# Optimization experiments

Hardware: AMD Instinct MI355X
Metric: run time of the kernel (lower is better)

Reference implementation:

```python
import jax, jax.numpy as jnp
import numpy as np

BUCKET_SIZE = 64
N_HASHES = 8
SELF_ATTN_VALUE = -5e4  # TOKEN_SELF_ATTN_VALUE
EPS = 1e-12  # F.normalize eps


def setup_inputs() -> dict:
    key = jax.random.key(0)
    k1, k2, k3 = jax.random.split(key, 3)
    B, S, D = 16, 4096, 128
    n_buckets = S // BUCKET_SIZE  # 64
    qk = jax.random.normal(k1, (B, S, D), dtype=jnp.float32)
    v = jax.random.normal(k2, (B, S, D), dtype=jnp.float32)
    # rotations_shape = (1, dim, n_hashes, n_buckets // 2); shared across batch
    rotations = jax.random.normal(k3, (1, D, N_HASHES, n_buckets // 2), dtype=jnp.float32)
    return {"qk": qk, "v": v, "rotations": rotations}


def _hash_vectors(qk, rotations, n_buckets):
    # qk: (B,S,D), rotations: (1,D,H,n_buckets//2)
    rotated = jnp.einsum('btf,fhi->bhti', qk, rotations[0])  # (B,H,S,nb/2)
    rotated = jnp.concatenate([rotated, -rotated], axis=-1)   # (B,H,S,nb)
    buckets = jnp.argmax(rotated, axis=-1)                    # (B,H,S)
    offsets = (jnp.arange(N_HASHES) * n_buckets)[None, :, None]
    return (buckets + offsets).reshape(qk.shape[0], -1)       # (B, H*S)


def _look_one_back(x):
    # concat each chunk with its predecessor (circular), along the window dim
    return jnp.concatenate([x, jnp.roll(x, 1, axis=1)], axis=2)


def reference(qk, v, rotations):
    B, S, D = qk.shape
    H = N_HASHES
    n_buckets = S // BUCKET_SIZE
    buckets = _hash_vectors(qk, rotations, n_buckets)         # (B, H*S) int

    ticker = jnp.broadcast_to(jnp.arange(H * S)[None, :], (B, H * S))
    buckets_and_t = S * buckets + (ticker % S)                # unique keys
    sticker = jnp.argsort(buckets_and_t, axis=-1)             # sort by bucket
    undo_sort = jnp.argsort(sticker, axis=-1)

    st = sticker % S                                          # original positions
    sqk = jnp.take_along_axis(qk, st[..., None], axis=1)      # (B,H*S,D)
    sv = jnp.take_along_axis(v, st[..., None], axis=1)

    C = H * n_buckets                                         # num chunks
    bq_t = st.reshape(B, C, -1)                               # (B,C,w)
    bqk = sqk.reshape(B, C, -1, D)
    bv = sv.reshape(B, C, -1, D)
    bq = bqk
    nrm = jnp.maximum(jnp.linalg.norm(bqk, axis=-1, keepdims=True), EPS)
    bk = bqk / nrm                                            # F.normalize

    bk = _look_one_back(bk)                                   # (B,C,2w,D)
    bv = _look_one_back(bv)
    bkv_t = _look_one_back(bq_t)                              # (B,C,2w)

    dots = jnp.einsum('bcie,bcje->bcij', bq, bk) * (D ** -0.5)  # (B,C,w,2w)
    self_mask = bq_t[:, :, :, None] == bkv_t[:, :, None, :]
    dots = jnp.where(self_mask, SELF_ATTN_VALUE, dots)

    lse = jax.scipy.special.logsumexp(dots, axis=-1, keepdims=True)
    probs = jnp.exp(dots - lse)
    bo = jnp.einsum('bcij,bcje->bcie', probs, bv)             # (B,C,w,D)

    so = bo.reshape(B, -1, D)                                 # (B,H*S,D)
    slogits = lse.reshape(B, -1)                              # (B,H*S)
    o = jnp.take_along_axis(so, undo_sort[..., None], axis=1)
    logits = jnp.take_along_axis(slogits, undo_sort, axis=1)

    o = o.reshape(B, H, S, D)
    logits = logits.reshape(B, H, S, 1)
    w = jnp.exp(logits - jax.scipy.special.logsumexp(logits, axis=1, keepdims=True))
    out = jnp.sum(o * w, axis=1)                              # (B,S,D)
    return out
```

## Files before the change

### kernel.cpp

```cpp
#include <hip/hip_runtime.h>
#include <hip/hip_bf16.h>


#define B_ 16
#define S_ 4096
#define D_ 128
#define H_ 8
#define C_ 512
#define SCALE_ 0.08838834764831845f

typedef __attribute__((ext_vector_type(8))) short bf16x8;
typedef __attribute__((ext_vector_type(8))) _Float16 f16x8;
typedef __attribute__((ext_vector_type(2))) _Float16 f16x2t;
typedef __attribute__((ext_vector_type(4))) float f32x4;
typedef __attribute__((ext_vector_type(2))) float f32x2v;
typedef __attribute__((ext_vector_type(4))) int int4v;

union BF8U { int4v i; bf16x8 b; };
union F16x8U { int4v i; f16x8 h; };

__device__ __forceinline__ unsigned hi_pack(float x0, float x1) {
    unsigned a, b;
    __builtin_memcpy(&b, &x0, 4);
    __builtin_memcpy(&a, &x1, 4);
    return __builtin_amdgcn_perm(a, b, 0x07060302u);
}
__device__ __forceinline__ float truncbf(float x) {
    unsigned u; __builtin_memcpy(&u, &x, 4);
    u &= 0xFFFF0000u;
    float f; __builtin_memcpy(&f, &u, 4);
    return f;
}
__device__ __forceinline__ unsigned pack2f16(float x0, float x1) {
    f16x2t h = {(_Float16)x0, (_Float16)x1};
    unsigned u; __builtin_memcpy(&u, &h, 4);
    return u;
}

__global__ __launch_bounds__(256) void norm_kernel(const float* __restrict__ qk,
                                                   float* __restrict__ rnrm) {
    int half = threadIdx.x >> 5;
    int lane32 = threadIdx.x & 31;
    size_t row = (size_t)blockIdx.x * 8 + half;
    float4 vv = ((const float4*)(qk + row * D_))[lane32];
    float ss = vv.x * vv.x + vv.y * vv.y + vv.z * vv.z + vv.w * vv.w;
    #pragma unroll
    for (int m = 1; m < 32; m <<= 1) ss += __shfl_xor(ss, m, 64);
    if (lane32 == 0) rnrm[row] = 1.0f / fmaxf(sqrtf(ss), 1e-12f);
}

__global__ __launch_bounds__(256) void prep_rot_kernel(const float* __restrict__ rot,
                                                       short* __restrict__ rth,
                                                       short* __restrict__ rtl) {
    int x = blockIdx.x * 256 + threadIdx.x;
    int hp = x >> 11;
    int ia = (x >> 5) & 63;
    int ft = x & 31;
    float v0 = rot[(size_t)(ft * 4 + 0) * 256 + hp * 64 + ia];
    float v1 = rot[(size_t)(ft * 4 + 1) * 256 + hp * 64 + ia];
    float v2 = rot[(size_t)(ft * 4 + 2) * 256 + hp * 64 + ia];
    float v3 = rot[(size_t)(ft * 4 + 3) * 256 + hp * 64 + ia];
    unsigned h0 = hi_pack(v0, v1), h1 = hi_pack(v2, v3);
    unsigned l0 = hi_pack(v0 - truncbf(v0), v1 - truncbf(v1));
    unsigned l1 = hi_pack(v2 - truncbf(v2), v3 - truncbf(v3));
    int off = ia * 128 + ((((ft >> 1) ^ (ia & 7)) << 3) | ((ft & 1) << 2));
    *(int2*)&rth[hp * 8192 + off] = make_int2((int)h0, (int)h1);
    *(int2*)&rtl[hp * 8192 + off] = make_int2((int)l0, (int)l1);
}

__global__ __launch_bounds__(256) void hash_kernel(const float* __restrict__ qk,
                                                   const float* __restrict__ rot,
                                                   const short* __restrict__ rth,
                                                   const short* __restrict__ rtl,
                                                   int* __restrict__ buckets) {
    __shared__ unsigned char flags[8][64];

    const int b = blockIdx.x >> 6;
    const int tile = blockIdx.x & 63;
    const int tid = threadIdx.x;
    const int w = tid >> 6, l = tid & 63, g = l >> 4, m = l & 15;

    if (tid < 32) ((int4*)flags)[tid] = make_int4(0, 0, 0, 0);
    __syncthreads();

    const float* qrow = qk + ((size_t)b * S_ + (size_t)tile * 64 + w * 16 + m) * D_;
    bf16x8 qh[4], qlr[4];
    #pragma unroll
    for (int s = 0; s < 4; ++s) {
        float4 xa = *(const float4*)(qrow + s * 32 + g * 8);
        float4 xb = *(const float4*)(qrow + s * 32 + g * 8 + 4);
        BF8U hu, lu;
        hu.i[0] = (int)hi_pack(xa.x, xa.y); hu.i[1] = (int)hi_pack(xa.z, xa.w);
        hu.i[2] = (int)hi_pack(xb.x, xb.y); hu.i[3] = (int)hi_pack(xb.z, xb.w);
        lu.i[0] = (int)hi_pack(xa.x - truncbf(xa.x), xa.y - truncbf(xa.y));
        lu.i[1] = (int)hi_pack(xa.z - truncbf(xa.z), xa.w - truncbf(xa.w));
        lu.i[2] = (int)hi_pack(xb.x - truncbf(xb.x), xb.y - truncbf(xb.y));
        lu.i[3] = (int)hi_pack(xb.z - truncbf(xb.z), xb.w - truncbf(xb.w));
        qh[s] = hu.b; qlr[s] = lu.b;
    }

    #pragma unroll
    for (int hp = 0; hp < 4; ++hp) {
        f32x4 dots_n[4];
        #pragma unroll
        for (int nt = 0; nt < 4; ++nt) {
            f32x4 acc = (f32x4){0.f, 0.f, 0.f, 0.f};
            #pragma unroll
            for (int s = 0; s < 4; ++s) {
                int kr = hp * 8192 + (nt * 16 + m) * 128 + (((s * 4 + g) ^ (m & 7)) << 3);
                bf16x8 bh = *(const bf16x8*)&rth[kr];
                bf16x8 bl = *(const bf16x8*)&rtl[kr];
                acc = __builtin_amdgcn_mfma_f32_16x16x32_bf16(qh[s], bh, acc, 0, 0, 0);
                acc = __builtin_amdgcn_mfma_f32_16x16x32_bf16(qh[s], bl, acc, 0, 0, 0);
                acc = __builtin_amdgcn_mfma_f32_16x16x32_bf16(qlr[s], bh, acc, 0, 0, 0);
            }
            dots_n[nt] = acc;
        }

        #pragma unroll
        for (int hh = 0; hh < 2; ++hh) {
            int h = hp * 2 + hh;
            #pragma unroll
            for (int r = 0; r < 4; ++r) {
                float v1 = -1e30f, v2 = -1e30f; int i1 = 0;
                #pragma unroll
                for (int nn = 0; nn < 2; ++nn) {
                    float v = dots_n[hh * 2 + nn][r];
                    int i = nn * 16 + m;
                    if (v > v1 || (v == v1 && i < i1)) { v2 = v1; v1 = v; i1 = i; }
                    else v2 = fmaxf(v2, v);
                    float nv = -v; int ni = i + 32;
                    if (nv > v1 || (nv == v1 && ni < i1)) { v2 = v1; v1 = nv; i1 = ni; }
                    else v2 = fmaxf(v2, nv);
                }
                #pragma unroll
                for (int mask = 1; mask <= 8; mask <<= 1) {
                    float ov1 = __shfl_xor(v1, mask, 64);
                    int   oi1 = __shfl_xor(i1, mask, 64);
                    float ov2 = __shfl_xor(v2, mask, 64);
                    bool takeOther = (ov1 > v1) || (ov1 == v1 && oi1 < i1);
                    float loser = takeOther ? v1 : ov1;
                    float nv1 = takeOther ? ov1 : v1;
                    int   ni1 = takeOther ? oi1 : i1;
                    v2 = fmaxf(fmaxf(v2, ov2), loser);
                    v1 = nv1; i1 = ni1;
                }
                if (m == 0) {
                    int tok = w * 16 + g * 4 + r;
                    if (v1 - v2 < 2e-2f) flags[h][tok] = 1;
                    buckets[(((size_t)(b * H_ + h)) << 12) + tile * 64 + tok] = i1;
                }
            }
        }
    }
    __syncthreads();

    int tok = tid >> 2, part = tid & 3;
    const float* qtok = qk + ((size_t)b * S_ + (size_t)tile * 64 + tok) * D_;
    for (int h = 0; h < H_; ++h) {
        if (!flags[h][tok]) continue;
        double pd[8] = {0, 0, 0, 0, 0, 0, 0, 0};
        #pragma unroll 2
        for (int f = 0; f < 128; ++f) {
            double q = (double)qtok[f];
            const float* rp = rot + (size_t)f * 256 + h * 32 + part * 8;
            float4 r0 = *(const float4*)rp;
            float4 r1 = *(const float4*)(rp + 4);
            pd[0] = fma(q, (double)r0.x, pd[0]);
            pd[1] = fma(q, (double)r0.y, pd[1]);
            pd[2] = fma(q, (double)r0.z, pd[2]);
            pd[3] = fma(q, (double)r0.w, pd[3]);
            pd[4] = fma(q, (double)r1.x, pd[4]);
            pd[5] = fma(q, (double)r1.y, pd[5]);
            pd[6] = fma(q, (double)r1.z, pd[6]);
            pd[7] = fma(q, (double)r1.w, pd[7]);
        }
        double bv = -1e300; int bi = 0;
        #pragma unroll
        for (int ii = 0; ii < 8; ++ii) {
            int i = part * 8 + ii;
            double v = pd[ii];
            if (v > bv || (v == bv && i < bi)) { bv = v; bi = i; }
            double nv = -v; int ni = i + 32;
            if (nv > bv || (nv == bv && ni < bi)) { bv = nv; bi = ni; }
        }
        #pragma unroll
        for (int mm = 1; mm <= 2; mm <<= 1) {
            double ov = __shfl_xor(bv, mm, 64);
            int oi = __shfl_xor(bi, mm, 64);
            if (ov > bv || (ov == bv && oi < bi)) { bv = ov; bi = oi; }
        }
        if (part == 0) buckets[(((size_t)(b * H_ + h)) << 12) + tile * 64 + tok] = bi;
    }
}

__global__ __launch_bounds__(256) void sort_kernel(const int* __restrict__ buckets,
                                                   int* __restrict__ st,
                                                   int* __restrict__ inv,
                                                   const float* __restrict__ rnrm,
                                                   float* __restrict__ rnrm_s) {
    __shared__ unsigned short hist[256][64];
    __shared__ int base[64];
    __shared__ int totals[64];
    int tid = threadIdx.x;
    const int* bkrow = buckets + (size_t)blockIdx.x * S_;
    const float* rnb = rnrm + (size_t)(blockIdx.x >> 3) * S_;

    unsigned int* h32 = (unsigned int*)hist;
    #pragma unroll
    for (int u = 0; u < 32; ++u) h32[u * 256 + tid] = 0;
    __syncthreads();

    #pragma unroll
    for (int u = 0; u < 16; ++u) {
        int t = tid * 16 + u;
        int bk = bkrow[t];
        hist[tid][bk]++;
    }
    __syncthreads();

    if (tid < 64) {
        int bucket = tid;
        int run = 0;
        for (int ch = 0; ch < 256; ++ch) {
            int v = hist[ch][bucket];
            hist[ch][bucket] = (unsigned short)run;
            run += v;
        }
        totals[bucket] = run;
    }
    __syncthreads();
    if (tid == 0) {
        int acc = 0;
        for (int k = 0; k < 64; ++k) { base[k] = acc; acc += totals[k]; }
    }
    __syncthreads();

    int* strow = st + (size_t)blockIdx.x * S_;
    int* invrow = inv + (size_t)blockIdx.x * S_;
    float* rnsrow = rnrm_s + (size_t)blockIdx.x * S_;
    #pragma unroll
    for (int u = 0; u < 16; ++u) {
        int t = tid * 16 + u;
        int bk = bkrow[t];
        int off = hist[tid][bk];
        hist[tid][bk] = (unsigned short)(off + 1);
        int pos = base[bk] + off;
        strow[pos] = t;
        invrow[t] = pos;
        rnsrow[pos] = rnb[t] * SCALE_;
    }
}

__device__ __forceinline__ void transpose4(const float4 v, int g, float (&w_)[4]) {
    bool b0 = (g & 1) != 0, b1 = (g & 2) != 0;
    float k0 = b1 ? v.z : v.x;
    float k1 = b1 ? v.w : v.y;
    float s0 = b1 ? v.x : v.z;
    float s1 = b1 ? v.y : v.w;
    float r0 = __shfl_xor(s0, 32, 64);
    float r1 = __shfl_xor(s1, 32, 64);
    float kq_ = b0 ? k1 : k0;
    float rq_ = b0 ? r1 : r0;
    float sk  = b0 ? k0 : k1;
    float sr  = b0 ? r0 : r1;
    float tk_ = __shfl_xor(sk, 16, 64);
    float tr_ = __shfl_xor(sr, 16, 64);
    float A0 = b0 ? tk_ : kq_;
    float A1 = b0 ? kq_ : tk_;
    float B0 = b0 ? tr_ : rq_;
    float B1 = b0 ? rq_ : tr_;
    w_[0] = b1 ? B0 : A0;
    w_[1] = b1 ? B1 : A1;
    w_[2] = b1 ? A0 : B0;
    w_[3] = b1 ? A1 : B1;
}

template<bool DENSE>
__global__ __launch_bounds__(256, 4) void attn_mfma_kernel(
        const float* __restrict__ qk, const float* __restrict__ rnrm_s,
        const float* __restrict__ vglob, const int* __restrict__ st,
        float* __restrict__ outnum, float* __restrict__ den,
        _Float16* __restrict__ snum, float* __restrict__ sden) {
    __shared__ int tq_s[64];
    __shared__ int tk1_s[64];
    __shared__ float rns0[64];
    __shared__ float rns1[64];
    __shared__ short kbuf[8192];
    __shared__ short vbuf[8192];

    const int p = blockIdx.x;
    const int bc = (p & 7) * 1024 + (p >> 3);
    const int b  = bc >> 9;
    const int c  = bc & 511;
    const int tid = threadIdx.x;
    const int w   = tid >> 6;
    const int l   = tid & 63;
    const int g   = l >> 4;
    const int m   = l & 15;
    const size_t bS = ((size_t)b << 12);
    const int* stb = st + ((size_t)b << 15);

    const int c1 = (c + 511) & 511;
    if (tid < 64) {
        tq_s[tid]  = stb[c * 64 + tid];
        tk1_s[tid] = stb[c1 * 64 + tid];
        rns0[tid] = rnrm_s[(((size_t)(b * H_ + (c >> 6))) << 12) + (size_t)(c & 63) * 64 + tid];
        rns1[tid] = rnrm_s[(((size_t)(b * H_ + (c1 >> 6))) << 12) + (size_t)(c1 & 63) * 64 + tid];
    }
    __syncthreads();

    const int qtok_m = tq_s[w * 16 + m];

    f16x8 qh[4];
    f32x4 e4[4];
    f32x4 acc_o[8];
    #pragma unroll
    for (int dt = 0; dt < 8; ++dt) acc_o[dt] = (f32x4){0.f, 0.f, 0.f, 0.f};
    float densum = 0.0f;

    float4 kreg[8];
    float4 va[4], vb[4];

    auto issue_k = [&](const int* __restrict__ toks) {
        #pragma unroll
        for (int u = 0; u < 8; ++u) {
            int token = u * 8 + (tid >> 5);
            int cc = tid & 31;
            kreg[u] = *(const float4*)(qk + (bS + toks[token]) * D_ + cc * 4);
        }
    };
    auto write_k = [&]() {
        #pragma unroll
        for (int u = 0; u < 8; ++u) {
            int token = u * 8 + (tid >> 5);
            int cc = tid & 31;
            float4 vv = kreg[u];
            unsigned h0 = pack2f16(vv.x, vv.y), h1 = pack2f16(vv.z, vv.w);
            int kw = token * 128 + ((((cc >> 1) ^ (token & 7)) << 3) | ((cc & 1) << 2));
            *(int2*)&kbuf[kw] = make_int2((int)h0, (int)h1);
        }
    };
    auto issue_v = [&](const int* __restrict__ toks) {
        #pragma unroll
        for (int up = 0; up < 4; ++up) {
            int kq8 = w * 16 + (up & 1) * 8;
            int cc = (up >> 1) * 16 + m;
            va[up] = *(const float4*)(vglob + (bS + toks[kq8 + g]) * D_ + cc * 4);
            vb[up] = *(const float4*)(vglob + (bS + toks[kq8 + 4 + g]) * D_ + cc * 4);
        }
    };
    auto write_v = [&]() {
        #pragma unroll
        for (int up = 0; up < 4; ++up) {
            int kq8 = w * 16 + (up & 1) * 8;
            int cc = (up >> 1) * 16 + m;
            float wa[4], wb[4];
            transpose4(va[up], g, wa);
            transpose4(vb[up], g, wb);
            unsigned h0 = pack2f16(wa[0], wa[1]), h1 = pack2f16(wa[2], wa[3]);
            unsigned h2 = pack2f16(wb[0], wb[1]), h3 = pack2f16(wb[2], wb[3]);
            int d = cc * 4 + g;
            int ds = d ^ ((d >> 3) & 7);
            int kg = kq8 >> 3;
            int idx = (kg * 128 + ds) * 8;
            *(int4*)&vbuf[idx] = make_int4((int)h0, (int)h1, (int)h2, (int)h3);
        }
    };
    auto qk_pass = [&](int mode, const float* __restrict__ rns,
                       const int* __restrict__ tkp) {
        #pragma unroll
        for (int kt = 0; kt < 4; ++kt) {
            f32x4 acc = (f32x4){0.f, 0.f, 0.f, 0.f};
            #pragma unroll
            for (int s4 = 0; s4 < 4; ++s4) {
                int kr = (kt * 16 + m) * 128 + (((s4 * 4 + g) ^ (m & 7)) << 3);
                f16x8 ah = *(const f16x8*)&kbuf[kr];
                acc = __builtin_amdgcn_mfma_f32_16x16x32_f16(ah, qh[s4], acc, 0, 0, 0);
            }
            f32x4 rn4 = *(const f32x4*)&rns[kt * 16 + g * 4];
            int4v kt4;
            if (mode == 1) kt4 = *(const int4v*)&tkp[kt * 16 + g * 4];
            f32x4 e;
            #pragma unroll
            for (int r = 0; r < 4; ++r) {
                float ev = __expf(acc[r] * rn4[r]);
                if (mode == 0) {
                    if (kt == w && (g * 4 + r) == m) ev = 0.0f;
                } else {
                    if (kt4[r] == qtok_m) ev = 0.0f;
                }
                e[r] = ev;
                densum += ev;
            }
            e4[kt] = e;
        }
    };
    auto pv_pass = [&]() {
        #pragma unroll
        for (int s = 0; s < 2; ++s) {
            float pav[8];
            #pragma unroll
            for (int c2 = 0; c2 < 2; ++c2) {
                int srcLane = ((g & 1) * 2 + c2) * 16 + m;
                #pragma unroll
                for (int r = 0; r < 4; ++r) {
                    float v0 = __shfl(e4[2 * s][r], srcLane, 64);
                    float v1 = __shfl(e4[2 * s + 1][r], srcLane, 64);
                    pav[c2 * 4 + r] = (g >> 1) ? v1 : v0;
                }
            }
            F16x8U pahu;
            #pragma unroll
            for (int j2 = 0; j2 < 4; ++j2)
                pahu.i[j2] = (int)pack2f16(pav[2 * j2], pav[2 * j2 + 1]);
            f16x8 pah = pahu.h;
            #pragma unroll
            for (int dt = 0; dt < 8; ++dt) {
                int d = dt * 16 + m;
                int ds = d ^ ((d >> 3) & 7);
                int base = ((s * 4 + g) * 128 + ds) * 8;
                f16x8 vh = *(const f16x8*)&vbuf[base];
                acc_o[dt] = __builtin_amdgcn_mfma_f32_16x16x32_f16(pah, vh, acc_o[dt], 0, 0, 0);
            }
        }
    };

    issue_k(tq_s);
    write_k();
    __syncthreads();

    #pragma unroll
    for (int s4 = 0; s4 < 4; ++s4) {
        int qr = (w * 16 + m) * 128 + (((s4 * 4 + g) ^ (m & 7)) << 3);
        qh[s4] = *(const f16x8*)&kbuf[qr];
    }
    issue_v(tq_s);
    qk_pass(0, rns0, tq_s);
    write_v();
    __syncthreads();

    issue_k(tk1_s);
    pv_pass();
    write_k();
    __syncthreads();

    issue_v(tk1_s);
    qk_pass(1, rns1, tk1_s);
    write_v();
    __syncthreads();

    pv_pass();

    densum += __shfl_xor(densum, 16, 64);
    densum += __shfl_xor(densum, 32, 64);

    if (DENSE) {
        const int h = c >> 6;
        const size_t base = (((size_t)(b * H_ + h)) << 12) + (size_t)(c & 63) * 64;
        #pragma unroll
        for (int r = 0; r < 4; ++r) {
            int row = w * 16 + g * 4 + r;
            _Float16* nrow = snum + (base + row) * D_;
            #pragma unroll
            for (int dt = 0; dt < 8; ++dt)
                __builtin_nontemporal_store((_Float16)acc_o[dt][r], nrow + dt * 16 + m);
        }
        if (g == 0) __builtin_nontemporal_store(densum, sden + base + w * 16 + m);
    } else {
        if (g == 0) atomicAdd(den + bS + qtok_m, densum);
        int4v q4tok = *(const int4v*)&tq_s[w * 16 + g * 4];
        #pragma unroll
        for (int r = 0; r < 4; ++r) {
            float* obase = outnum + ((bS + q4tok[r]) * D_);
            #pragma unroll
            for (int dt = 0; dt < 8; ++dt)
                atomicAdd(obase + dt * 16 + m, acc_o[dt][r]);
        }
    }
}

__global__ __launch_bounds__(256) void combine_kernel(
        const _Float16* __restrict__ snum, const float* __restrict__ sden,
        const int* __restrict__ inv, float* __restrict__ out) {
    int wv = threadIdx.x >> 6, l = threadIdx.x & 63;
    int t = blockIdx.x * 4 + wv;
    int b = t >> 12, s = t & 4095;
    float s0 = 0.f, s1 = 0.f, dsum = 0.f;
    #pragma unroll
    for (int h = 0; h < H_; ++h) {
        int bh = b * H_ + h;
        int pos = inv[((size_t)bh << 12) + s];
        size_t row = ((size_t)bh << 12) + pos;
        dsum += __builtin_nontemporal_load(sden + row);
        unsigned uv = __builtin_nontemporal_load(
            (const unsigned*)(snum + row * D_ + 2 * l));
        unsigned short us0 = (unsigned short)(uv & 0xFFFFu);
        unsigned short us1 = (unsigned short)(uv >> 16);
        _Float16 h0, h1;
        __builtin_memcpy(&h0, &us0, 2);
        __builtin_memcpy(&h1, &us1, 2);
        s0 += (float)h0;
        s1 += (float)h1;
    }
    float rd = 1.0f / dsum;
    f32x2v o2 = {s0 * rd, s1 * rd};
    __builtin_nontemporal_store(o2, (f32x2v*)(out + (size_t)t * D_ + 2 * l));
}

__global__ __launch_bounds__(256) void div_kernel(float* __restrict__ out,
                                                  const float* __restrict__ den) {
    int i = blockIdx.x * 256 + threadIdx.x;
    float4 o = ((float4*)out)[i];
    float dn = den[i >> 5];
    ((float4*)out)[i] = make_float4(o.x / dn, o.y / dn, o.z / dn, o.w / dn);
}

extern "C" void kernel_launch(void* const* d_in, const int* in_sizes, int n_in,
                              void* d_out, int out_size, void* d_ws, size_t ws_size,
                              hipStream_t stream) {
    const float* qk  = (const float*)d_in[0];
    const float* v   = (const float*)d_in[1];
    const float* rot = (const float*)d_in[2];
    float* out = (float*)d_out;

    char* ws = (char*)d_ws;
    float* rnrm    = (float*)ws;
    int* buckets   = (int*)(ws + 262144);
    int* inv       = buckets;
    int* st        = (int*)(ws + 2359296);
    float* rnrm_s  = (float*)(ws + 4456448);
    float* sden    = (float*)(ws + 6553600);
    short* rth     = (short*)(ws + 8650752);
    short* rtl     = (short*)(ws + 8716288);
    _Float16* snum = (_Float16*)(ws + 8781824);
    const size_t need = 8781824ull + 134217728ull;

    norm_kernel<<<B_ * S_ / 8, 256, 0, stream>>>(qk, rnrm);
    prep_rot_kernel<<<32, 256, 0, stream>>>(rot, rth, rtl);
    hash_kernel<<<B_ * (S_ / 64), 256, 0, stream>>>(qk, rot, rth, rtl, buckets);
    sort_kernel<<<B_ * H_, 256, 0, stream>>>(buckets, st, inv, rnrm, rnrm_s);

    if (ws_size >= need) {
        attn_mfma_kernel<true><<<B_ * C_, 256, 0, stream>>>(
            qk, rnrm_s, v, st, nullptr, nullptr, snum, sden);
        combine_kernel<<<B_ * S_ / 4, 256, 0, stream>>>(snum, sden, inv, out);
    } else {
        float* den = sden;
        hipMemsetAsync(out, 0, (size_t)B_ * S_ * D_ * 4, stream);
        hipMemsetAsync(den, 0, (size_t)B_ * S_ * 4, stream);
        attn_mfma_kernel<false><<<B_ * C_, 256, 0, stream>>>(
            qk, rnrm_s, v, st, out, den, nullptr, nullptr);
        div_kernel<<<B_ * S_ * D_ / 4 / 256, 256, 0, stream>>>(out, den);
    }
}
```

Before: 274.4 us.

## Split hash kernel across hash pairs and pack argmax into 64-bit keys

The hash kernel now launches four times as many blocks, each handling one pair of hashes for a 64-token tile instead of all eight hashes, which raises parallelism and lets occupancy hints apply. The top-2 argmax reduction is rewritten to use order-preserving 64-bit packed keys (value plus inverted index), so each shuffle step moves two 64-bit values instead of three separate float/int values and compares them without branches. The cost is that every block reloads and re-splits the same qk tile into bf16 hi/lo parts, so qk reads and conversion work are repeated four times.

```diff
diff --git a/kernel.cpp b/kernel.cpp
--- a/kernel.cpp
+++ b/kernel.cpp
@@ -35,6 +35,14 @@
     f16x2t h = {(_Float16)x0, (_Float16)x1};
     unsigned u; __builtin_memcpy(&u, &h, 4);
     return u;
+}
+__device__ __forceinline__ unsigned enc_ks(unsigned u) {
+    return (u & 0x80000000u) ? ~u : (u | 0x80000000u);
+}
+__device__ __forceinline__ float dec_ks(unsigned ks) {
+    unsigned u = (ks & 0x80000000u) ? (ks ^ 0x80000000u) : ~ks;
+    float f; __builtin_memcpy(&f, &u, 4);
+    return f;
 }
 
 __global__ __launch_bounds__(256) void norm_kernel(const float* __restrict__ qk,
@@ -68,19 +76,20 @@
     *(int2*)&rtl[hp * 8192 + off] = make_int2((int)l0, (int)l1);
 }
 
-__global__ __launch_bounds__(256) void hash_kernel(const float* __restrict__ qk,
-                                                   const float* __restrict__ rot,
-                                                   const short* __restrict__ rth,
-                                                   const short* __restrict__ rtl,
-                                                   int* __restrict__ buckets) {
-    __shared__ unsigned char flags[8][64];
-
-    const int b = blockIdx.x >> 6;
-    const int tile = blockIdx.x & 63;
+__global__ __launch_bounds__(256, 4) void hash_kernel(
+        const float* __restrict__ qk, const float* __restrict__ rot,
+        const short* __restrict__ rth, const short* __restrict__ rtl,
+        int* __restrict__ buckets) {
+    __shared__ unsigned char flags[2][64];
+
+    const int bid = blockIdx.x;
+    const int b = bid >> 8;
+    const int tile = (bid >> 2) & 63;
+    const int hp = bid & 3;
     const int tid = threadIdx.x;
     const int w = tid >> 6, l = tid & 63, g = l >> 4, m = l & 15;
 
-    if (tid < 32) ((int4*)flags)[tid] = make_int4(0, 0, 0, 0);
+    if (tid < 8) ((int4*)flags)[tid] = make_int4(0, 0, 0, 0);
     __syncthreads();
 
     const float* qrow = qk + ((size_t)b * S_ + (size_t)tile * 64 + w * 16 + m) * D_;
@@ -99,57 +108,57 @@
         qh[s] = hu.b; qlr[s] = lu.b;
     }
 
-    #pragma unroll
-    for (int hp = 0; hp < 4; ++hp) {
-        f32x4 dots_n[4];
-        #pragma unroll
-        for (int nt = 0; nt < 4; ++nt) {
-            f32x4 acc = (f32x4){0.f, 0.f, 0.f, 0.f};
-            #pragma unroll
-            for (int s = 0; s < 4; ++s) {
-                int kr = hp * 8192 + (nt * 16 + m) * 128 + (((s * 4 + g) ^ (m & 7)) << 3);
-                bf16x8 bh = *(const bf16x8*)&rth[kr];
-                bf16x8 bl = *(const bf16x8*)&rtl[kr];
-                acc = __builtin_amdgcn_mfma_f32_16x16x32_bf16(qh[s], bh, acc, 0, 0, 0);
-                acc = __builtin_amdgcn_mfma_f32_16x16x32_bf16(qh[s], bl, acc, 0, 0, 0);
-                acc = __builtin_amdgcn_mfma_f32_16x16x32_bf16(qlr[s], bh, acc, 0, 0, 0);
-            }
-            dots_n[nt] = acc;
-        }
-
-        #pragma unroll
-        for (int hh = 0; hh < 2; ++hh) {
-            int h = hp * 2 + hh;
-            #pragma unroll
-            for (int r = 0; r < 4; ++r) {
-                float v1 = -1e30f, v2 = -1e30f; int i1 = 0;
-                #pragma unroll
-                for (int nn = 0; nn < 2; ++nn) {
-                    float v = dots_n[hh * 2 + nn][r];
-                    int i = nn * 16 + m;
-                    if (v > v1 || (v == v1 && i < i1)) { v2 = v1; v1 = v; i1 = i; }
-                    else v2 = fmaxf(v2, v);
-                    float nv = -v; int ni = i + 32;
-                    if (nv > v1 || (nv == v1 && ni < i1)) { v2 = v1; v1 = nv; i1 = ni; }
-                    else v2 = fmaxf(v2, nv);
-                }
-                #pragma unroll
-                for (int mask = 1; mask <= 8; mask <<= 1) {
-                    float ov1 = __shfl_xor(v1, mask, 64);
-                    int   oi1 = __shfl_xor(i1, mask, 64);
-                    float ov2 = __shfl_xor(v2, mask, 64);
-                    bool takeOther = (ov1 > v1) || (ov1 == v1 && oi1 < i1);
-                    float loser = takeOther ? v1 : ov1;
-                    float nv1 = takeOther ? ov1 : v1;
-                    int   ni1 = takeOther ? oi1 : i1;
-                    v2 = fmaxf(fmaxf(v2, ov2), loser);
-                    v1 = nv1; i1 = ni1;
-                }
-                if (m == 0) {
-                    int tok = w * 16 + g * 4 + r;
-                    if (v1 - v2 < 2e-2f) flags[h][tok] = 1;
-                    buckets[(((size_t)(b * H_ + h)) << 12) + tile * 64 + tok] = i1;
-                }
+    f32x4 dots_n[4];
+    #pragma unroll
+    for (int nt = 0; nt < 4; ++nt) {
+        f32x4 acc = (f32x4){0.f, 0.f, 0.f, 0.f};
+        #pragma unroll
+        for (int s = 0; s < 4; ++s) {
+            int kr = hp * 8192 + (nt * 16 + m) * 128 + (((s * 4 + g) ^ (m & 7)) << 3);
+            bf16x8 bh = *(const bf16x8*)&rth[kr];
+            bf16x8 bl = *(const bf16x8*)&rtl[kr];
+            acc = __builtin_amdgcn_mfma_f32_16x16x32_bf16(qh[s], bh, acc, 0, 0, 0);
+            acc = __builtin_amdgcn_mfma_f32_16x16x32_bf16(qh[s], bl, acc, 0, 0, 0);
+            acc = __builtin_amdgcn_mfma_f32_16x16x32_bf16(qlr[s], bh, acc, 0, 0, 0);
+        }
+        dots_n[nt] = acc;
+    }
+
+    #pragma unroll
+    for (int hh = 0; hh < 2; ++hh) {
+        int h = hp * 2 + hh;
+        #pragma unroll
+        for (int r = 0; r < 4; ++r) {
+            unsigned long long kM = 0ull, kS = 0ull;
+            #pragma unroll
+            for (int nn = 0; nn < 2; ++nn) {
+                float v = dots_n[hh * 2 + nn][r];
+                unsigned u; __builtin_memcpy(&u, &v, 4);
+                int i = nn * 16 + m;
+                unsigned long long kp =
+                    ((unsigned long long)enc_ks(u) << 6) | (unsigned)(63 - i);
+                unsigned long long kn =
+                    ((unsigned long long)enc_ks(u ^ 0x80000000u) << 6) |
+                    (unsigned)(63 - (i + 32));
+                if (kp > kM) { kS = kM; kM = kp; } else if (kp > kS) kS = kp;
+                if (kn > kM) { kS = kM; kM = kn; } else if (kn > kS) kS = kn;
+            }
+            #pragma unroll
+            for (int st = 1; st <= 8; st <<= 1) {
+                unsigned long long oM = __shfl_xor(kM, st, 64);
+                unsigned long long oS = __shfl_xor(kS, st, 64);
+                unsigned long long lo = kM < oM ? kM : oM;
+                kM = kM > oM ? kM : oM;
+                unsigned long long hs = kS > oS ? kS : oS;
+                kS = hs > lo ? hs : lo;
+            }
+            if (m == 0) {
+                int tok = w * 16 + g * 4 + r;
+                int i1 = 63 - (int)(kM & 63ull);
+                float v1 = dec_ks((unsigned)(kM >> 6));
+                float v2 = dec_ks((unsigned)(kS >> 6));
+                if (v1 - v2 < 2e-2f) flags[hh][tok] = 1;
+                buckets[(((size_t)(b * H_ + h)) << 12) + tile * 64 + tok] = i1;
             }
         }
     }
@@ -157,8 +166,9 @@
 
     int tok = tid >> 2, part = tid & 3;
     const float* qtok = qk + ((size_t)b * S_ + (size_t)tile * 64 + tok) * D_;
-    for (int h = 0; h < H_; ++h) {
-        if (!flags[h][tok]) continue;
+    for (int hh = 0; hh < 2; ++hh) {
+        if (!flags[hh][tok]) continue;
+        int h = hp * 2 + hh;
         double pd[8] = {0, 0, 0, 0, 0, 0, 0, 0};
         #pragma unroll 2
         for (int f = 0; f < 128; ++f) {
@@ -190,7 +200,8 @@
             int oi = __shfl_xor(bi, mm, 64);
             if (ov > bv || (ov == bv && oi < bi)) { bv = ov; bi = oi; }
         }
-        if (part == 0) buckets[(((size_t)(b * H_ + h)) << 12) + tile * 64 + tok] = bi;
+        if (part == 0)
+            buckets[(((size_t)(b * H_ + h)) << 12) + tile * 64 + tok] = bi;
     }
 }
 
@@ -538,7 +549,7 @@
 
     norm_kernel<<<B_ * S_ / 8, 256, 0, stream>>>(qk, rnrm);
     prep_rot_kernel<<<32, 256, 0, stream>>>(rot, rth, rtl);
-    hash_kernel<<<B_ * (S_ / 64), 256, 0, stream>>>(qk, rot, rth, rtl, buckets);
+    hash_kernel<<<B_ * (S_ / 64) * 4, 256, 0, stream>>>(qk, rot, rth, rtl, buckets);
     sort_kernel<<<B_ * H_, 256, 0, stream>>>(buckets, st, inv, rnrm, rnrm_s);
 
     if (ws_size >= need) {
```

Result: faster. 263.1 us (-4.1%).
